# Kernel tuning notes

Measured on AMD Instinct MI355X. Metric: run time of the kernel, lower is better.

The kernel has to match this reference:

```python
import jax, jax.numpy as jnp
import numpy as np

WINDOW = 50


def setup_inputs() -> dict:
    key = jax.random.key(0)
    ks = jax.random.split(key, 7)
    B, N = 32, 32768
    hidden = 32
    x = jax.random.normal(ks[0], (B, N), dtype=jnp.float32)
    # torch Linear weights stored as [in, out] (already transposed)
    w1 = jax.random.normal(ks[1], (4, 2 * hidden), dtype=jnp.float32) * (1.0 / np.sqrt(4))
    b1 = jnp.zeros((2 * hidden,), dtype=jnp.float32)
    w2 = jax.random.normal(ks[2], (2 * hidden, hidden), dtype=jnp.float32) * (1.0 / np.sqrt(2 * hidden))
    b2 = jnp.zeros((hidden,), dtype=jnp.float32)
    w3 = jax.random.normal(ks[3], (hidden, 2), dtype=jnp.float32) * (1.0 / np.sqrt(hidden))
    b3 = jnp.zeros((2,), dtype=jnp.float32)
    return {"x": x, "w1": w1, "b1": b1, "w2": w2, "b2": b2, "w3": w3, "b3": b3}


def reference(x, w1, b1, w2, b2, w3, b3):
    W = WINDOW
    B, N = x.shape
    M = N - W + 1
    # windows: [B, M, W] via gather (same layout as torch.unfold)
    idx = jnp.arange(M)[:, None] + jnp.arange(W)[None, :]  # [M, W]
    windows = x[:, idx]  # [B, M, W]
    mean = windows.mean(axis=-1, keepdims=True)
    centered = windows - mean
    # torch .std() is unbiased (ddof=1)
    var = (centered ** 2).sum(axis=-1, keepdims=True) / (W - 1)
    std = jnp.sqrt(var) + 1e-6
    skew = (centered ** 3).mean(axis=-1, keepdims=True) / std ** 3
    kurt = (centered ** 4).mean(axis=-1, keepdims=True) / std ** 4
    stats = jnp.concatenate([mean, std, skew, kurt], axis=-1)  # [B, M, 4]
    h = jax.nn.relu(stats @ w1 + b1)
    h = jax.nn.relu(h @ w2 + b2)
    params = h @ w3 + b3  # [B, M, 2]
    gamma = params[:, :, 0:1]
    beta = params[:, :, 1:2]
    normalized = centered / std
    reprojected = normalized * gamma + beta  # [B, M, W]
    return reprojected[:, :, W // 2]  # [B, M]
```

## Files before the change

### kernel.cpp

```cpp
#include <hip/hip_runtime.h>
#include <hip/hip_bf16.h>
#include <math.h>

#define WINDOW 50

typedef __attribute__((ext_vector_type(8))) short short8;
typedef __attribute__((ext_vector_type(4))) float f32x4;
typedef unsigned int uint;

union U8 { uint4 u; short8 s; };
__device__ inline short8 as_s8(uint4 u) { U8 t; t.u = u; return t.s; }

__device__ inline uint pk2(float a, float b) {
    uint r;
    asm("v_cvt_pk_bf16_f32 %0, %1, %2" : "=v"(r) : "v"(a), "v"(b));
    return r;
}
__device__ inline float lo_f32(uint u) { return __uint_as_float(u << 16); }
__device__ inline float hi_f32(uint u) { return __uint_as_float(u & 0xffff0000u); }

__global__ __launch_bounds__(256, 4) void nsg_kernel(
    const float* __restrict__ x,
    const float* __restrict__ w1, const float* __restrict__ b1,
    const float* __restrict__ w2, const float* __restrict__ b2,
    const float* __restrict__ w3, const float* __restrict__ b3,
    float* __restrict__ out, int N, int M, int tiles)
{
    __shared__ float s_x[564];
    __shared__ f32x4 s_buf[1088];
    __shared__ uint4 s_a2l[4][64];
    __shared__ uint4 s_stat[4][128];

    const int tid = threadIdx.x;
    const int wv  = tid >> 6;
    const int wl  = tid & 63;
    const int l15 = wl & 15;
    const int g   = wl >> 4;
    const int tile = blockIdx.x % tiles;
    const int row  = blockIdx.x / tiles;
    const int m0   = tile * 512;

    const float* xr = x + (size_t)row * N;
    for (int i = tid; i < 562; i += 256) {
        int gg = m0 + i;
        s_x[i] = (gg < N) ? xr[gg] : 0.0f;
    }

    short8 A1[4];
    #pragma unroll
    for (int nt = 0; nt < 4; ++nt) {
        int n = nt * 16 + l15;
        float a = w1[n], b = w1[64 + n], c = w1[128 + n], d = w1[192 + n];
        uint hab = pk2(a, b), hcd = pk2(c, d);
        uint lab = pk2(a - lo_f32(hab), b - hi_f32(hab));
        uint lcd = pk2(c - lo_f32(hcd), d - hi_f32(hcd));
        float bb = b1[n];
        uint bh = pk2(bb, 0.0f);
        uint bpk = pk2(bb, bb - lo_f32(bh));
        uint4 u;
        u.x = (g == 0) ? hab : (g == 1) ? lab : (g == 2) ? bpk : 0u;
        u.y = (g == 0) ? hcd : (g == 1) ? lcd : 0u;
        u.z = (g == 0) ? hab : (g == 1) ? lab : 0u;
        u.w = (g == 0) ? hcd : (g == 1) ? lcd : 0u;
        A1[nt] = as_s8(u);
    }

    uint4 A2h[2][2];
    #pragma unroll
    for (int mt = 0; mt < 2; ++mt) {
        int c = mt * 16 + l15;
        #pragma unroll
        for (int ks = 0; ks < 2; ++ks) {
            uint hu[4], lu[4];
            #pragma unroll
            for (int p = 0; p < 4; ++p) {
                int n = ks * 32 + g * 8 + 2 * p;
                float a = w2[n * 32 + c], b = w2[(n + 1) * 32 + c];
                uint h = pk2(a, b);
                hu[p] = h;
                lu[p] = pk2(a - lo_f32(h), b - hi_f32(h));
            }
            A2h[mt][ks] = make_uint4(hu[0], hu[1], hu[2], hu[3]);
            if (wv == 0) s_a2l[mt * 2 + ks][wl] = make_uint4(lu[0], lu[1], lu[2], lu[3]);
        }
    }

    f32x4 b2r[2];
    #pragma unroll
    for (int mt = 0; mt < 2; ++mt)
        b2r[mt] = *(const f32x4*)(b2 + 16 * mt + 4 * g);
    float2 w3r[8];
    #pragma unroll
    for (int mt = 0; mt < 2; ++mt)
        #pragma unroll
        for (int j = 0; j < 4; ++j)
            w3r[mt * 4 + j] = *(const float2*)(w3 + (16 * mt + 4 * g + j) * 2);
    const float b3g = b3[0], b3b = b3[1];

    __syncthreads();

    f32x4* s_chunk = s_buf;
    f32x4 myC[2];
    #pragma unroll
    for (int s = 0; s < 2; ++s) {
        int t = tid + 256 * s;
        float S1 = 0.f, S2 = 0.f, S3 = 0.f, S4 = 0.f;
        #pragma unroll
        for (int i = 0; i < 10; ++i) {
            float v = s_x[t + i], v2 = v * v;
            S1 += v; S2 += v2; S3 = fmaf(v2, v, S3); S4 = fmaf(v2, v2, S4);
        }
        myC[s] = f32x4{S1, S2, S3, S4};
        s_chunk[t] = myC[s];
    }
    if (tid < 40) {
        int t = tid + 512;
        float S1 = 0.f, S2 = 0.f, S3 = 0.f, S4 = 0.f;
        #pragma unroll
        for (int i = 0; i < 10; ++i) {
            float v = s_x[t + i], v2 = v * v;
            S1 += v; S2 += v2; S3 = fmaf(v2, v, S3); S4 = fmaf(v2, v2, S4);
        }
        s_chunk[t] = f32x4{S1, S2, S3, S4};
    }
    __syncthreads();

    float nrm[2];
    #pragma unroll
    for (int s = 0; s < 2; ++s) {
        int t = tid + 256 * s;
        f32x4 ca = s_chunk[t + 10], cb = s_chunk[t + 20];
        f32x4 cc = s_chunk[t + 30], cd = s_chunk[t + 40];
        float S1 = myC[s][0] + ca[0] + cb[0] + cc[0] + cd[0];
        float S2 = myC[s][1] + ca[1] + cb[1] + cc[1] + cd[1];
        float S3 = myC[s][2] + ca[2] + cb[2] + cc[2] + cd[2];
        float S4 = myC[s][3] + ca[3] + cb[3] + cc[3] + cd[3];
        const float invW = 1.0f / (float)WINDOW;
        float mean = S1 * invW;
        float mu2  = mean * mean;
        float c2m = S2 - (float)WINDOW * mu2;
        float c3m = S3 - 3.0f * mean * S2 + 2.0f * (float)WINDOW * mu2 * mean;
        float c4m = S4 - 4.0f * mean * S3 + 6.0f * mu2 * S2
                      - 3.0f * (float)WINDOW * mu2 * mu2;
        float var    = c2m * (1.0f / (float)(WINDOW - 1));
        float sd     = sqrtf(var) + 1e-6f;
        float inv_sd = 1.0f / sd;
        float inv_sd2 = inv_sd * inv_sd;
        float skew = c3m * invW * inv_sd2 * inv_sd;
        float kurt = c4m * invW * inv_sd2 * inv_sd2;
        uint h01 = pk2(mean, sd), h23 = pk2(skew, kurt);
        uint l01 = pk2(mean - lo_f32(h01), sd - hi_f32(h01));
        uint l23 = pk2(skew - lo_f32(h23), kurt - hi_f32(h23));
        s_stat[wv][s * 64 + wl] = make_uint4(h01, h23, l01, l23);
        nrm[s] = (s_x[t + 25] - mean) * inv_sd;
    }
    __syncthreads();

    uint* h1b = (uint*)(s_buf + wv * 272);
    const uint K2 = (g == 2) ? 0x3F803F80u : 0u;
    const bool gHi = (g >= 2);
    float ga[2] = {0.f, 0.f}, be[2] = {0.f, 0.f};

    #pragma unroll
    for (int q = 0; q < 8; ++q) {
        const int s = q >> 2, sub = q & 3;
        uint4 st = s_stat[wv][s * 64 + sub * 16 + l15];
        uint4 bq;
        bq.x = gHi ? K2 : st.x;
        bq.y = gHi ? 0u : st.y;
        bq.z = gHi ? 0u : st.z;
        bq.w = gHi ? 0u : st.w;
        short8 B1 = as_s8(bq);

        #pragma unroll
        for (int nt = 0; nt < 4; ++nt) {
            f32x4 c1 = f32x4{0.f, 0.f, 0.f, 0.f};
            c1 = __builtin_amdgcn_mfma_f32_16x16x32_bf16(A1[nt], B1, c1, 0, 0, 0);
            float r0 = fmaxf(c1[0], 0.f), r1 = fmaxf(c1[1], 0.f);
            float r2 = fmaxf(c1[2], 0.f), r3 = fmaxf(c1[3], 0.f);
            uint h01 = pk2(r0, r1), h23 = pk2(r2, r3);
            uint q01 = pk2(r0 - lo_f32(h01), r1 - hi_f32(h01));
            uint q23 = pk2(r2 - lo_f32(h23), r3 - hi_f32(h23));
            int d = l15 * 68 + 8 * nt + 2 * g;
            *(uint2*)&h1b[d]      = make_uint2(h01, h23);
            *(uint2*)&h1b[d + 32] = make_uint2(q01, q23);
        }
        __builtin_amdgcn_wave_barrier();

        short8 Bh0 = as_s8(*(uint4*)&h1b[l15 * 68 +  0 + 4 * g]);
        short8 Bh1 = as_s8(*(uint4*)&h1b[l15 * 68 + 16 + 4 * g]);
        short8 Bl0 = as_s8(*(uint4*)&h1b[l15 * 68 + 32 + 4 * g]);
        short8 Bl1 = as_s8(*(uint4*)&h1b[l15 * 68 + 48 + 4 * g]);

        float pg = 0.f, pb = 0.f;
        #pragma unroll
        for (int mt = 0; mt < 2; ++mt) {
            short8 a2l0 = as_s8(s_a2l[mt * 2 + 0][wl]);
            short8 a2l1 = as_s8(s_a2l[mt * 2 + 1][wl]);
            f32x4 c2 = b2r[mt];
            c2 = __builtin_amdgcn_mfma_f32_16x16x32_bf16(as_s8(A2h[mt][0]), Bh0, c2, 0, 0, 0);
            c2 = __builtin_amdgcn_mfma_f32_16x16x32_bf16(as_s8(A2h[mt][1]), Bh1, c2, 0, 0, 0);
            c2 = __builtin_amdgcn_mfma_f32_16x16x32_bf16(as_s8(A2h[mt][0]), Bl0, c2, 0, 0, 0);
            c2 = __builtin_amdgcn_mfma_f32_16x16x32_bf16(as_s8(A2h[mt][1]), Bl1, c2, 0, 0, 0);
            c2 = __builtin_amdgcn_mfma_f32_16x16x32_bf16(a2l0, Bh0, c2, 0, 0, 0);
            c2 = __builtin_amdgcn_mfma_f32_16x16x32_bf16(a2l1, Bh1, c2, 0, 0, 0);
            #pragma unroll
            for (int j = 0; j < 4; ++j) {
                float P = fmaxf(c2[j], 0.f);
                float2 w = w3r[mt * 4 + j];
                pg = fmaf(P, w.x, pg);
                pb = fmaf(P, w.y, pb);
            }
        }
        pg += __shfl_xor(pg, 16);
        pb += __shfl_xor(pb, 16);
        pg += __shfl_xor(pg, 32);
        pb += __shfl_xor(pb, 32);
        if (g == sub) { ga[s] = pg; be[s] = pb; }
    }

    #pragma unroll
    for (int s = 0; s < 2; ++s) {
        int m = m0 + tid + 256 * s;
        if (m < M)
            out[(size_t)row * M + m] = fmaf(nrm[s], ga[s] + b3g, be[s] + b3b);
    }
}

extern "C" void kernel_launch(void* const* d_in, const int* in_sizes, int n_in,
                              void* d_out, int out_size, void* d_ws, size_t ws_size,
                              hipStream_t stream) {
    const float* x  = (const float*)d_in[0];
    const float* w1 = (const float*)d_in[1];
    const float* b1 = (const float*)d_in[2];
    const float* w2 = (const float*)d_in[3];
    const float* b2 = (const float*)d_in[4];
    const float* w3 = (const float*)d_in[5];
    const float* b3 = (const float*)d_in[6];
    float* out = (float*)d_out;

    const int N = 32768;
    const int B = in_sizes[0] / N;
    const int M = N - WINDOW + 1;
    const int tiles = (M + 511) / 512;

    dim3 grid(B * tiles), block(256);
    nsg_kernel<<<grid, block, 0, stream>>>(x, w1, b1, w2, b2, w3, b3,
                                           out, N, M, tiles);
}
```

Before: 34.51 us.

## Loop each block over two 256-output tiles with shuffled stats and split MFMA chains

```diff
diff --git a/kernel.cpp b/kernel.cpp
--- a/kernel.cpp
+++ b/kernel.cpp
@@ -19,32 +19,22 @@
 __device__ inline float lo_f32(uint u) { return __uint_as_float(u << 16); }
 __device__ inline float hi_f32(uint u) { return __uint_as_float(u & 0xffff0000u); }
 
-__global__ __launch_bounds__(256, 4) void nsg_kernel(
+__global__ __launch_bounds__(256, 5) void nsg_kernel(
     const float* __restrict__ x,
     const float* __restrict__ w1, const float* __restrict__ b1,
     const float* __restrict__ w2, const float* __restrict__ b2,
     const float* __restrict__ w3, const float* __restrict__ b3,
-    float* __restrict__ out, int N, int M, int tiles)
+    float* __restrict__ out, int N, int M, int nunits)
 {
-    __shared__ float s_x[564];
-    __shared__ f32x4 s_buf[1088];
+    __shared__ float s_x[312];
+    __shared__ uint4 s_bufq[1088];
     __shared__ uint4 s_a2l[4][64];
-    __shared__ uint4 s_stat[4][128];
 
     const int tid = threadIdx.x;
     const int wv  = tid >> 6;
     const int wl  = tid & 63;
     const int l15 = wl & 15;
     const int g   = wl >> 4;
-    const int tile = blockIdx.x % tiles;
-    const int row  = blockIdx.x / tiles;
-    const int m0   = tile * 512;
-
-    const float* xr = x + (size_t)row * N;
-    for (int i = tid; i < 562; i += 256) {
-        int gg = m0 + i;
-        s_x[i] = (gg < N) ? xr[gg] : 0.0f;
-    }
 
     short8 A1[4];
     #pragma unroll
@@ -55,7 +45,7 @@
         uint lab = pk2(a - lo_f32(hab), b - hi_f32(hab));
         uint lcd = pk2(c - lo_f32(hcd), d - hi_f32(hcd));
         float bb = b1[n];
-        uint bh = pk2(bb, 0.0f);
+        uint bh  = pk2(bb, 0.0f);
         uint bpk = pk2(bb, bb - lo_f32(bh));
         uint4 u;
         u.x = (g == 0) ? hab : (g == 1) ? lab : (g == 2) ? bpk : 0u;
@@ -64,7 +54,6 @@
         u.w = (g == 0) ? hcd : (g == 1) ? lcd : 0u;
         A1[nt] = as_s8(u);
     }
-
     uint4 A2h[2][2];
     #pragma unroll
     for (int mt = 0; mt < 2; ++mt) {
@@ -84,7 +73,6 @@
             if (wv == 0) s_a2l[mt * 2 + ks][wl] = make_uint4(lu[0], lu[1], lu[2], lu[3]);
         }
     }
-
     f32x4 b2r[2];
     #pragma unroll
     for (int mt = 0; mt < 2; ++mt)
@@ -96,45 +84,57 @@
         for (int j = 0; j < 4; ++j)
             w3r[mt * 4 + j] = *(const float2*)(w3 + (16 * mt + 4 * g + j) * 2);
     const float b3g = b3[0], b3b = b3[1];
+    const uint  K2  = (g == 2) ? 0x3F803F80u : 0u;
+    const bool  gHi = (g >= 2);
+
+    uint* h1b = (uint*)(s_bufq + 272 * wv);
+    f32x4* s_chunk = (f32x4*)s_bufq;
 
     __syncthreads();
 
-    f32x4* s_chunk = s_buf;
-    f32x4 myC[2];
-    #pragma unroll
-    for (int s = 0; s < 2; ++s) {
-        int t = tid + 256 * s;
-        float S1 = 0.f, S2 = 0.f, S3 = 0.f, S4 = 0.f;
-        #pragma unroll
-        for (int i = 0; i < 10; ++i) {
-            float v = s_x[t + i], v2 = v * v;
-            S1 += v; S2 += v2; S3 = fmaf(v2, v, S3); S4 = fmaf(v2, v2, S4);
-        }
-        myC[s] = f32x4{S1, S2, S3, S4};
-        s_chunk[t] = myC[s];
-    }
-    if (tid < 40) {
-        int t = tid + 512;
-        float S1 = 0.f, S2 = 0.f, S3 = 0.f, S4 = 0.f;
-        #pragma unroll
-        for (int i = 0; i < 10; ++i) {
-            float v = s_x[t + i], v2 = v * v;
-            S1 += v; S2 += v2; S3 = fmaf(v2, v, S3); S4 = fmaf(v2, v2, S4);
-        }
-        s_chunk[t] = f32x4{S1, S2, S3, S4};
-    }
-    __syncthreads();
-
-    float nrm[2];
-    #pragma unroll
-    for (int s = 0; s < 2; ++s) {
-        int t = tid + 256 * s;
-        f32x4 ca = s_chunk[t + 10], cb = s_chunk[t + 20];
-        f32x4 cc = s_chunk[t + 30], cd = s_chunk[t + 40];
-        float S1 = myC[s][0] + ca[0] + cb[0] + cc[0] + cd[0];
-        float S2 = myC[s][1] + ca[1] + cb[1] + cc[1] + cd[1];
-        float S3 = myC[s][2] + ca[2] + cb[2] + cc[2] + cd[2];
-        float S4 = myC[s][3] + ca[3] + cb[3] + cc[3] + cd[3];
+    #pragma unroll 1
+    for (int k = 0; k < 2; ++k) {
+        int u = 2 * (int)blockIdx.x + k;
+        if (u >= nunits) break;
+        const int row = u >> 7;
+        const int m0  = (u & 127) * 256;
+        const float* xr = x + (size_t)row * N;
+
+        for (int i = tid; i < 306; i += 256) {
+            int gg = m0 + i;
+            s_x[i] = (gg < N) ? xr[gg] : 0.0f;
+        }
+        __syncthreads();
+
+        f32x4 myC;
+        {
+            float S1 = 0.f, S2 = 0.f, S3 = 0.f, S4 = 0.f;
+            #pragma unroll
+            for (int i = 0; i < 10; ++i) {
+                float v = s_x[tid + i], v2 = v * v;
+                S1 += v; S2 += v2; S3 = fmaf(v2, v, S3); S4 = fmaf(v2, v2, S4);
+            }
+            myC = f32x4{S1, S2, S3, S4};
+            s_chunk[tid] = myC;
+        }
+        if (tid < 40) {
+            int t = tid + 256;
+            float S1 = 0.f, S2 = 0.f, S3 = 0.f, S4 = 0.f;
+            #pragma unroll
+            for (int i = 0; i < 10; ++i) {
+                float v = s_x[t + i], v2 = v * v;
+                S1 += v; S2 += v2; S3 = fmaf(v2, v, S3); S4 = fmaf(v2, v2, S4);
+            }
+            s_chunk[t] = f32x4{S1, S2, S3, S4};
+        }
+        __syncthreads();
+
+        f32x4 ca = s_chunk[tid + 10], cb = s_chunk[tid + 20];
+        f32x4 cc = s_chunk[tid + 30], cd = s_chunk[tid + 40];
+        float S1 = myC[0] + ca[0] + cb[0] + cc[0] + cd[0];
+        float S2 = myC[1] + ca[1] + cb[1] + cc[1] + cd[1];
+        float S3 = myC[2] + ca[2] + cb[2] + cc[2] + cd[2];
+        float S4 = myC[3] + ca[3] + cb[3] + cc[3] + cd[3];
         const float invW = 1.0f / (float)WINDOW;
         float mean = S1 * invW;
         float mu2  = mean * mean;
@@ -148,82 +148,85 @@
         float inv_sd2 = inv_sd * inv_sd;
         float skew = c3m * invW * inv_sd2 * inv_sd;
         float kurt = c4m * invW * inv_sd2 * inv_sd2;
-        uint h01 = pk2(mean, sd), h23 = pk2(skew, kurt);
-        uint l01 = pk2(mean - lo_f32(h01), sd - hi_f32(h01));
-        uint l23 = pk2(skew - lo_f32(h23), kurt - hi_f32(h23));
-        s_stat[wv][s * 64 + wl] = make_uint4(h01, h23, l01, l23);
-        nrm[s] = (s_x[t + 25] - mean) * inv_sd;
-    }
-    __syncthreads();
-
-    uint* h1b = (uint*)(s_buf + wv * 272);
-    const uint K2 = (g == 2) ? 0x3F803F80u : 0u;
-    const bool gHi = (g >= 2);
-    float ga[2] = {0.f, 0.f}, be[2] = {0.f, 0.f};
-
-    #pragma unroll
-    for (int q = 0; q < 8; ++q) {
-        const int s = q >> 2, sub = q & 3;
-        uint4 st = s_stat[wv][s * 64 + sub * 16 + l15];
-        uint4 bq;
-        bq.x = gHi ? K2 : st.x;
-        bq.y = gHi ? 0u : st.y;
-        bq.z = gHi ? 0u : st.z;
-        bq.w = gHi ? 0u : st.w;
-        short8 B1 = as_s8(bq);
-
+        float nrm  = (s_x[tid + 25] - mean) * inv_sd;
+
+        uint4 stp;
+        {
+            uint h01 = pk2(mean, sd), h23 = pk2(skew, kurt);
+            stp.x = h01;
+            stp.y = h23;
+            stp.z = pk2(mean - lo_f32(h01), sd - hi_f32(h01));
+            stp.w = pk2(skew - lo_f32(h23), kurt - hi_f32(h23));
+        }
+        __syncthreads();
+
+        float ga = 0.f, be = 0.f;
         #pragma unroll
-        for (int nt = 0; nt < 4; ++nt) {
-            f32x4 c1 = f32x4{0.f, 0.f, 0.f, 0.f};
-            c1 = __builtin_amdgcn_mfma_f32_16x16x32_bf16(A1[nt], B1, c1, 0, 0, 0);
-            float r0 = fmaxf(c1[0], 0.f), r1 = fmaxf(c1[1], 0.f);
-            float r2 = fmaxf(c1[2], 0.f), r3 = fmaxf(c1[3], 0.f);
-            uint h01 = pk2(r0, r1), h23 = pk2(r2, r3);
-            uint q01 = pk2(r0 - lo_f32(h01), r1 - hi_f32(h01));
-            uint q23 = pk2(r2 - lo_f32(h23), r3 - hi_f32(h23));
-            int d = l15 * 68 + 8 * nt + 2 * g;
-            *(uint2*)&h1b[d]      = make_uint2(h01, h23);
-            *(uint2*)&h1b[d + 32] = make_uint2(q01, q23);
-        }
-        __builtin_amdgcn_wave_barrier();
-
-        short8 Bh0 = as_s8(*(uint4*)&h1b[l15 * 68 +  0 + 4 * g]);
-        short8 Bh1 = as_s8(*(uint4*)&h1b[l15 * 68 + 16 + 4 * g]);
-        short8 Bl0 = as_s8(*(uint4*)&h1b[l15 * 68 + 32 + 4 * g]);
-        short8 Bl1 = as_s8(*(uint4*)&h1b[l15 * 68 + 48 + 4 * g]);
-
-        float pg = 0.f, pb = 0.f;
-        #pragma unroll
-        for (int mt = 0; mt < 2; ++mt) {
-            short8 a2l0 = as_s8(s_a2l[mt * 2 + 0][wl]);
-            short8 a2l1 = as_s8(s_a2l[mt * 2 + 1][wl]);
-            f32x4 c2 = b2r[mt];
-            c2 = __builtin_amdgcn_mfma_f32_16x16x32_bf16(as_s8(A2h[mt][0]), Bh0, c2, 0, 0, 0);
-            c2 = __builtin_amdgcn_mfma_f32_16x16x32_bf16(as_s8(A2h[mt][1]), Bh1, c2, 0, 0, 0);
-            c2 = __builtin_amdgcn_mfma_f32_16x16x32_bf16(as_s8(A2h[mt][0]), Bl0, c2, 0, 0, 0);
-            c2 = __builtin_amdgcn_mfma_f32_16x16x32_bf16(as_s8(A2h[mt][1]), Bl1, c2, 0, 0, 0);
-            c2 = __builtin_amdgcn_mfma_f32_16x16x32_bf16(a2l0, Bh0, c2, 0, 0, 0);
-            c2 = __builtin_amdgcn_mfma_f32_16x16x32_bf16(a2l1, Bh1, c2, 0, 0, 0);
-            #pragma unroll
-            for (int j = 0; j < 4; ++j) {
-                float P = fmaxf(c2[j], 0.f);
-                float2 w = w3r[mt * 4 + j];
-                pg = fmaf(P, w.x, pg);
-                pb = fmaf(P, w.y, pb);
-            }
-        }
-        pg += __shfl_xor(pg, 16);
-        pb += __shfl_xor(pb, 16);
-        pg += __shfl_xor(pg, 32);
-        pb += __shfl_xor(pb, 32);
-        if (g == sub) { ga[s] = pg; be[s] = pb; }
-    }
-
-    #pragma unroll
-    for (int s = 0; s < 2; ++s) {
-        int m = m0 + tid + 256 * s;
+        for (int q = 0; q < 4; ++q) {
+            const int src = q * 16 + l15;
+            uint4 st;
+            st.x = __shfl(stp.x, src, 64);
+            st.y = __shfl(stp.y, src, 64);
+            st.z = __shfl(stp.z, src, 64);
+            st.w = __shfl(stp.w, src, 64);
+            uint4 bq;
+            bq.x = gHi ? K2 : st.x;
+            bq.y = gHi ? 0u : st.y;
+            bq.z = gHi ? 0u : st.z;
+            bq.w = gHi ? 0u : st.w;
+            short8 B1 = as_s8(bq);
+
+            #pragma unroll
+            for (int nt = 0; nt < 4; ++nt) {
+                f32x4 c1 = f32x4{0.f, 0.f, 0.f, 0.f};
+                c1 = __builtin_amdgcn_mfma_f32_16x16x32_bf16(A1[nt], B1, c1, 0, 0, 0);
+                float r0 = fmaxf(c1[0], 0.f), r1 = fmaxf(c1[1], 0.f);
+                float r2 = fmaxf(c1[2], 0.f), r3 = fmaxf(c1[3], 0.f);
+                uint h01 = pk2(r0, r1), h23 = pk2(r2, r3);
+                uint q01 = pk2(r0 - lo_f32(h01), r1 - hi_f32(h01));
+                uint q23 = pk2(r2 - lo_f32(h23), r3 - hi_f32(h23));
+                int d = l15 * 68 + 8 * nt + 2 * g;
+                *(uint2*)&h1b[d]      = make_uint2(h01, h23);
+                *(uint2*)&h1b[d + 32] = make_uint2(q01, q23);
+            }
+            __builtin_amdgcn_wave_barrier();
+
+            short8 Bh0 = as_s8(*(uint4*)&h1b[l15 * 68 +  0 + 4 * g]);
+            short8 Bh1 = as_s8(*(uint4*)&h1b[l15 * 68 + 16 + 4 * g]);
+            short8 Bl0 = as_s8(*(uint4*)&h1b[l15 * 68 + 32 + 4 * g]);
+            short8 Bl1 = as_s8(*(uint4*)&h1b[l15 * 68 + 48 + 4 * g]);
+
+            float pg = 0.f, pb = 0.f;
+            #pragma unroll
+            for (int mt = 0; mt < 2; ++mt) {
+                short8 a2l0 = as_s8(s_a2l[mt * 2 + 0][wl]);
+                short8 a2l1 = as_s8(s_a2l[mt * 2 + 1][wl]);
+                f32x4 c2a = b2r[mt];
+                c2a = __builtin_amdgcn_mfma_f32_16x16x32_bf16(as_s8(A2h[mt][0]), Bh0, c2a, 0, 0, 0);
+                c2a = __builtin_amdgcn_mfma_f32_16x16x32_bf16(as_s8(A2h[mt][1]), Bh1, c2a, 0, 0, 0);
+                c2a = __builtin_amdgcn_mfma_f32_16x16x32_bf16(a2l0, Bh0, c2a, 0, 0, 0);
+                f32x4 c2b = f32x4{0.f, 0.f, 0.f, 0.f};
+                c2b = __builtin_amdgcn_mfma_f32_16x16x32_bf16(as_s8(A2h[mt][0]), Bl0, c2b, 0, 0, 0);
+                c2b = __builtin_amdgcn_mfma_f32_16x16x32_bf16(as_s8(A2h[mt][1]), Bl1, c2b, 0, 0, 0);
+                c2b = __builtin_amdgcn_mfma_f32_16x16x32_bf16(a2l1, Bh1, c2b, 0, 0, 0);
+                #pragma unroll
+                for (int j = 0; j < 4; ++j) {
+                    float P = fmaxf(c2a[j] + c2b[j], 0.f);
+                    float2 w = w3r[mt * 4 + j];
+                    pg = fmaf(P, w.x, pg);
+                    pb = fmaf(P, w.y, pb);
+                }
+            }
+            pg += __shfl_xor(pg, 16);
+            pb += __shfl_xor(pb, 16);
+            pg += __shfl_xor(pg, 32);
+            pb += __shfl_xor(pb, 32);
+            if (g == q) { ga = pg; be = pb; }
+        }
+
+        int m = m0 + tid;
         if (m < M)
-            out[(size_t)row * M + m] = fmaf(nrm[s], ga[s] + b3g, be[s] + b3b);
+            out[(size_t)row * M + m] = fmaf(nrm, ga + b3g, be + b3b);
     }
 }
 
@@ -240,11 +243,10 @@
     float* out = (float*)d_out;
 
     const int N = 32768;
-    const int B = in_sizes[0] / N;
     const int M = N - WINDOW + 1;
-    const int tiles = (M + 511) / 512;
-
-    dim3 grid(B * tiles), block(256);
+    const int nunits = 32 * 128;
+
+    dim3 grid(2048), block(256);
     nsg_kernel<<<grid, block, 0, stream>>>(x, w1, b1, w2, b2, w3, b3,
-                                           out, N, M, tiles);
+                                           out, N, M, nunits);
 }
```

New measurement: 81.25 us. +135.5%, slower.
